# Kernel optimization log

Measured on AMD Instinct MI355X. Metric: run time of the kernel, lower is better.

## Reference

```python
import jax, jax.numpy as jnp
import numpy as np

NSAMPLE = 8
IN_FEAT = 64

def setup_inputs() -> dict:
    key = jax.random.key(0)
    ks = jax.random.split(key, 8)
    B, N1, N2, C = 2, 4096, 16384, IN_FEAT
    xyz1 = jax.random.normal(ks[0], (B, 3, N1), jnp.float32)
    xyz2 = jax.random.normal(ks[1], (B, 3, N2), jnp.float32)
    feat1 = jax.random.normal(ks[2], (B, C, N1), jnp.float32)
    flow = jax.random.normal(ks[3], (B, 3, N1), jnp.float32)
    W1 = jax.random.normal(ks[4], (C, C + 3), jnp.float32) * 0.1
    b1 = jax.random.normal(ks[5], (C,), jnp.float32) * 0.1
    W2 = jax.random.normal(ks[6], (3, C), jnp.float32) * 0.1
    b2 = jax.random.normal(ks[7], (3,), jnp.float32) * 0.1
    return {"xyz1": xyz1, "xyz2": xyz2, "feat1": feat1, "flow": flow,
            "W1": W1, "b1": b1, "W2": W2, "b2": b2}

def _knn_idx(xyz2, xyz1, k):
    # squared distances between queries xyz2 [B,3,N2] and targets xyz1 [B,3,N1]
    q2 = jnp.sum(xyz2 * xyz2, axis=1)            # [B,N2]
    t2 = jnp.sum(xyz1 * xyz1, axis=1)            # [B,N1]
    qt = jnp.einsum('bcn,bcm->bnm', xyz2, xyz1)  # [B,N2,N1]
    d = q2[:, :, None] + t2[:, None, :] - 2.0 * qt
    _, idx = jax.lax.top_k(-d, k)                # [B,N2,k] nearest in N1
    return idx

def _group(x, idx):
    # x [B,C,N1], idx [B,N2,k] -> [B,C,N2,k]
    return jax.vmap(lambda xb, ib: xb[:, ib])(x, idx)

def reference(xyz1, xyz2, feat1, flow, W1, b1, W2, b2):
    idx = _knn_idx(xyz2, xyz1, NSAMPLE)
    group_flow = _group(flow, idx)                           # [B,3,N2,k]
    group_xyz = _group(xyz1, idx) - xyz2[:, :, :, None]      # [B,3,N2,k]
    group_feat = _group(feat1, idx)                          # [B,C,N2,k]
    h = jnp.concatenate([group_feat, group_xyz], axis=1)     # [B,C+3,N2,k]
    h = jnp.einsum('oc,bcnk->bonk', W1, h) + b1[None, :, None, None]
    h = jnp.where(h >= 0, h, 0.1 * h)                        # LeakyReLU(0.1)
    w = jnp.einsum('oc,bcnk->bonk', W2, h) + b2[None, :, None, None]  # [B,3,N2,k]
    w = jax.nn.softmax(w, axis=3)
    up_flow = jnp.sum(group_flow * w, axis=3)                # [B,3,N2]
    return up_flow
```

## Files before the change

kernel.cpp:

```cpp
#include <hip/hip_runtime.h>
#include <cstdint>
#include <cstddef>

#define NB    2
#define N1    4096
#define N2    16384
#define CF    64
#define KNN   8
#define SPLIT1 16
#define NS1   (N1 / SPLIT1)
#define NQ    (NB * N2)

#define DNET(d) do { \
    const float m0_ = fminf(d, d0); \
    const float m1_ = __builtin_amdgcn_fmed3f(d, d0, d1); \
    const float m2_ = __builtin_amdgcn_fmed3f(d, d1, d2); \
    const float m3_ = __builtin_amdgcn_fmed3f(d, d2, d3); \
    const float m4_ = __builtin_amdgcn_fmed3f(d, d3, d4); \
    const float m5_ = __builtin_amdgcn_fmed3f(d, d4, d5); \
    const float m6_ = __builtin_amdgcn_fmed3f(d, d5, d6); \
    const float m7_ = __builtin_amdgcn_fmed3f(d, d6, d7); \
    d0=m0_; d1=m1_; d2=m2_; d3=m3_; d4=m4_; d5=m5_; d6=m6_; d7=m7_; \
} while (0)

__device__ __forceinline__ float distq(float qx, float qy, float qz, float q2,
                                       float4 p) {
    const float qt = __fadd_rn(
        __fadd_rn(__fmul_rn(qx, p.x), __fmul_rn(qy, p.y)),
        __fmul_rn(qz, p.z));
    return __fsub_rn(__fadd_rn(q2, p.w), __fadd_rn(qt, qt));
}

__global__ __launch_bounds__(256, 2) void k_pack(
    const float* __restrict__ xyz1, const float* __restrict__ xyz2,
    const float* __restrict__ feat1, const float* __restrict__ flow,
    float* __restrict__ feat1T, float4* __restrict__ aux4,
    float4* __restrict__ flow4, float4* __restrict__ q4)
{
    __shared__ float tile[64][65];
    const int b  = blockIdx.y;
    const int n0 = blockIdx.x * 64;
    const int tid = threadIdx.x;
    const int nl = tid & 63, cq = tid >> 6;

#pragma unroll
    for (int r = 0; r < 16; ++r) {
        const int c = r * 4 + cq;
        tile[c][nl] = feat1[((size_t)(b * CF + c)) * N1 + n0 + nl];
    }
    __syncthreads();
#pragma unroll
    for (int r = 0; r < 16; ++r) {
        const int nn = r * 4 + cq;
        feat1T[((size_t)(b * N1 + n0 + nn)) * CF + nl] = tile[nl][nn];
    }
    if (tid < 64) {
        const int n = n0 + tid;
        const float x = xyz1[(b * 3 + 0) * N1 + n];
        const float y = xyz1[(b * 3 + 1) * N1 + n];
        const float z = xyz1[(b * 3 + 2) * N1 + n];
        const float t2 = __fadd_rn(__fadd_rn(__fmul_rn(x, x), __fmul_rn(y, y)),
                                   __fmul_rn(z, z));
        aux4[b * N1 + n] = make_float4(x, y, z, t2);
        const float fx = flow[(b * 3 + 0) * N1 + n];
        const float fy = flow[(b * 3 + 1) * N1 + n];
        const float fz = flow[(b * 3 + 2) * N1 + n];
        flow4[b * N1 + n] = make_float4(fx, fy, fz, 0.f);
    }
    {
        const int qid = (blockIdx.y * 64 + blockIdx.x) * 256 + tid;
        const int qb_ = qid >> 14, qn_ = qid & (N2 - 1);
        const float x = xyz2[(qb_ * 3 + 0) * N2 + qn_];
        const float y = xyz2[(qb_ * 3 + 1) * N2 + qn_];
        const float z = xyz2[(qb_ * 3 + 2) * N2 + qn_];
        const float q2 = __fadd_rn(__fadd_rn(__fmul_rn(x, x), __fmul_rn(y, y)),
                                   __fmul_rn(z, z));
        q4[qid] = make_float4(x, y, z, q2);
    }
}

__global__ __launch_bounds__(256, 4) void k_knn5(
    const float4* __restrict__ aux4, const float4* __restrict__ q4,
    float* __restrict__ partd)
{
    __shared__ float4 pts[NS1];
    const int sp  = blockIdx.y;
    const int tid = threadIdx.x;
    const int qa  = blockIdx.x * 512 + tid;
    const int qb  = qa + 256;
    const int b   = qa >> 14;

    if (tid < NS1) {
        pts[tid] = aux4[b * N1 + sp * NS1 + tid];
    }
    __syncthreads();

    const float4 A = q4[qa];
    const float4 C = q4[qb];
    const float ax = A.x, ay = A.y, az = A.z, a2 = A.w;
    const float cx = C.x, cy = C.y, cz = C.z, c2 = C.w;

    float Aq0=INFINITY,Aq1=INFINITY,Aq2=INFINITY,Aq3=INFINITY,
          Aq4=INFINITY,Aq5=INFINITY,Aq6=INFINITY,Aq7=INFINITY;
    float Bq0=INFINITY,Bq1=INFINITY,Bq2=INFINITY,Bq3=INFINITY,
          Bq4=INFINITY,Bq5=INFINITY,Bq6=INFINITY,Bq7=INFINITY;

#pragma unroll 4
    for (int j = 0; j < NS1; ++j) {
        const float4 p = pts[j];
        const float dA = distq(ax, ay, az, a2, p);
        const float dB = distq(cx, cy, cz, c2, p);
        {
            float d0=Aq0,d1=Aq1,d2=Aq2,d3=Aq3,d4=Aq4,d5=Aq5,d6=Aq6,d7=Aq7;
            DNET(dA);
            Aq0=d0;Aq1=d1;Aq2=d2;Aq3=d3;Aq4=d4;Aq5=d5;Aq6=d6;Aq7=d7;
        }
        {
            float d0=Bq0,d1=Bq1,d2=Bq2,d3=Bq3,d4=Bq4,d5=Bq5,d6=Bq6,d7=Bq7;
            DNET(dB);
            Bq0=d0;Bq1=d1;Bq2=d2;Bq3=d3;Bq4=d4;Bq5=d5;Bq6=d6;Bq7=d7;
        }
    }

    {
        float4* pd4 = (float4*)(partd + ((size_t)sp * NQ + qa) * KNN);
        pd4[0] = make_float4(Aq0, Aq1, Aq2, Aq3);
        pd4[1] = make_float4(Aq4, Aq5, Aq6, Aq7);
    }
    {
        float4* pd4 = (float4*)(partd + ((size_t)sp * NQ + qb) * KNN);
        pd4[0] = make_float4(Bq0, Bq1, Bq2, Bq3);
        pd4[1] = make_float4(Bq4, Bq5, Bq6, Bq7);
    }
}

__global__ __launch_bounds__(256, 2) void k_thr(
    const float* __restrict__ partd, float* __restrict__ thr,
    int* __restrict__ tneed, int* __restrict__ smask)
{
    const int q = blockIdx.x * 256 + threadIdx.x;
    float d0=INFINITY,d1=INFINITY,d2=INFINITY,d3=INFINITY,
          d4=INFINITY,d5=INFINITY,d6=INFINITY,d7=INFINITY;
    float mn[SPLIT1];

#pragma unroll
    for (int sp = 0; sp < SPLIT1; ++sp) {
        const float4* pd4 = (const float4*)(partd + ((size_t)sp * NQ + q) * KNN);
        const float4 lo = pd4[0], hi = pd4[1];
        mn[sp] = lo.x;
        { const float d = lo.x; DNET(d); }
        { const float d = lo.y; DNET(d); }
        { const float d = lo.z; DNET(d); }
        { const float d = lo.w; DNET(d); }
        { const float d = hi.x; DNET(d); }
        { const float d = hi.y; DNET(d); }
        { const float d = hi.z; DNET(d); }
        { const float d = hi.w; DNET(d); }
    }
    const int s = (d0 < d7) + (d1 < d7) + (d2 < d7) + (d3 < d7) +
                  (d4 < d7) + (d5 < d7) + (d6 < d7);
    int mask = 0;
#pragma unroll
    for (int sp = 0; sp < SPLIT1; ++sp)
        mask |= (mn[sp] <= d7) ? (1 << sp) : 0;

    thr[q]   = d7;
    tneed[q] = 8 - s;
    smask[q] = mask;
}

__global__ __launch_bounds__(256, 4) void k_sel5(
    const float4* __restrict__ aux4, const float4* __restrict__ q4,
    const float* __restrict__ thr, const int* __restrict__ tneed,
    const int* __restrict__ smask, int* __restrict__ knn_idx)
{
    const int tid  = threadIdx.x;
    const int wave = tid >> 6, lane = tid & 63;
    const int q    = blockIdx.x * 4 + wave;
    const int b    = q >> 14;

    const float4 qv   = q4[q];
    const float  thrq = thr[q];
    const int    tn   = tneed[q];
    int mask = smask[q];

    int pos = 0, tc = 0;
    int* ko = knn_idx + (size_t)q * KNN;
    const float4* pts = aux4 + b * N1;

    while (mask) {
        const int sp = __builtin_ctz(mask); mask &= mask - 1;
        const int jb = sp * NS1;
#pragma unroll
        for (int t = 0; t < 4; ++t) {
            const float4 p = pts[jb + t * 64 + lane];
            const float d = distq(qv.x, qv.y, qv.z, qv.w, p);
            unsigned long long s = __ballot(d <  thrq);
            unsigned long long e = __ballot(d == thrq);
            const int jbase = jb + t * 64;
            while (s) {
                const int bit = __builtin_ctzll(s); s &= s - 1;
                if (lane == 0 && pos < 8) ko[pos] = jbase + bit;
                ++pos;
            }
            while (e && tc < tn) {
                const int bit = __builtin_ctzll(e); e &= e - 1;
                if (lane == 0 && pos < 8) ko[pos] = jbase + bit;
                ++pos; ++tc;
            }
        }
        if (pos >= 8) break;
    }
}

#define R4(WV, C4, BK) { \
    const float4 i0_ = *(const float4*)(inw + ((BK)+0)*68 + (C4)*4); \
    const float4 i1_ = *(const float4*)(inw + ((BK)+1)*68 + (C4)*4); \
    const float4 i2_ = *(const float4*)(inw + ((BK)+2)*68 + (C4)*4); \
    const float4 i3_ = *(const float4*)(inw + ((BK)+3)*68 + (C4)*4); \
    ha = fmaf((WV).x, i0_.x, ha); ha = fmaf((WV).y, i0_.y, ha); \
    ha = fmaf((WV).z, i0_.z, ha); ha = fmaf((WV).w, i0_.w, ha); \
    hb = fmaf((WV).x, i1_.x, hb); hb = fmaf((WV).y, i1_.y, hb); \
    hb = fmaf((WV).z, i1_.z, hb); hb = fmaf((WV).w, i1_.w, hb); \
    hc = fmaf((WV).x, i2_.x, hc); hc = fmaf((WV).y, i2_.y, hc); \
    hc = fmaf((WV).z, i2_.z, hc); hc = fmaf((WV).w, i2_.w, hc); \
    hd = fmaf((WV).x, i3_.x, hd); hd = fmaf((WV).y, i3_.y, hd); \
    hd = fmaf((WV).z, i3_.z, hd); hd = fmaf((WV).w, i3_.w, hd); \
}

#define DPPS12(PRE, MODS, POST) \
    asm(PRE \
        "v_add_f32_dpp %0, %0, %0 "   MODS "\n\t" \
        "v_add_f32_dpp %1, %1, %1 "   MODS "\n\t" \
        "v_add_f32_dpp %2, %2, %2 "   MODS "\n\t" \
        "v_add_f32_dpp %3, %3, %3 "   MODS "\n\t" \
        "v_add_f32_dpp %4, %4, %4 "   MODS "\n\t" \
        "v_add_f32_dpp %5, %5, %5 "   MODS "\n\t" \
        "v_add_f32_dpp %6, %6, %6 "   MODS "\n\t" \
        "v_add_f32_dpp %7, %7, %7 "   MODS "\n\t" \
        "v_add_f32_dpp %8, %8, %8 "   MODS "\n\t" \
        "v_add_f32_dpp %9, %9, %9 "   MODS "\n\t" \
        "v_add_f32_dpp %10, %10, %10 " MODS "\n\t" \
        "v_add_f32_dpp %11, %11, %11 " MODS POST \
        : "+v"(pa0), "+v"(pb0), "+v"(pc0), "+v"(pd0), \
          "+v"(pa1), "+v"(pb1), "+v"(pc1), "+v"(pd1), \
          "+v"(pa2), "+v"(pb2), "+v"(pc2), "+v"(pd2))

#define RDL(v) __int_as_float(__builtin_amdgcn_readlane(__float_as_int(v), 63))

#define L1L2_QUAD(BK, SA0,SA1,SA2,SA3, SB0,SB1,SB2,SB3, SC0,SC1,SC2,SC3) do { \
    float ha = b1v, hb = b1v, hc = b1v, hd = b1v; \
    R4(w0, 0, BK)  R4(w1, 1, BK)  R4(w2, 2, BK)  R4(w3, 3, BK) \
    R4(w4, 4, BK)  R4(w5, 5, BK)  R4(w6, 6, BK)  R4(w7, 7, BK) \
    R4(w8, 8, BK)  R4(w9, 9, BK)  R4(w10,10, BK) R4(w11,11, BK) \
    R4(w12,12, BK) R4(w13,13, BK) R4(w14,14, BK) R4(w15,15, BK) \
    R4(w16,16, BK) \
    ha = ha >= 0.f ? ha : 0.1f * ha; \
    hb = hb >= 0.f ? hb : 0.1f * hb; \
    hc = hc >= 0.f ? hc : 0.1f * hc; \
    hd = hd >= 0.f ? hd : 0.1f * hd; \
    float pa0 = w2a*ha, pb0 = w2a*hb, pc0 = w2a*hc, pd0 = w2a*hd; \
    float pa1 = w2b*ha, pb1 = w2b*hb, pc1 = w2b*hc, pd1 = w2b*hd; \
    float pa2 = w2c*ha, pb2 = w2c*hb, pc2 = w2c*hc, pd2 = w2c*hd; \
    DPPS12("s_nop 1\n\t", "row_shr:1 row_mask:0xf bank_mask:0xf", ""); \
    DPPS12("", "row_shr:2 row_mask:0xf bank_mask:0xf", ""); \
    DPPS12("", "row_shr:4 row_mask:0xf bank_mask:0xf", ""); \
    DPPS12("", "row_shr:8 row_mask:0xf bank_mask:0xf", ""); \
    DPPS12("", "row_bcast:15 row_mask:0xa bank_mask:0xf", ""); \
    DPPS12("", "row_bcast:31 row_mask:0xc bank_mask:0xf", "\n\ts_nop 1"); \
    SA0 = RDL(pa0) + b20; SA1 = RDL(pb0) + b20; \
    SA2 = RDL(pc0) + b20; SA3 = RDL(pd0) + b20; \
    SB0 = RDL(pa1) + b21; SB1 = RDL(pb1) + b21; \
    SB2 = RDL(pc1) + b21; SB3 = RDL(pd1) + b21; \
    SC0 = RDL(pa2) + b22; SC1 = RDL(pb2) + b22; \
    SC2 = RDL(pc2) + b22; SC3 = RDL(pd2) + b22; \
} while (0)

#define SMAX8(sa, sb, sc, sd, se, sf, sg, sh, CH, res) do { \
    const float m_ = fmaxf(fmaxf(fmaxf(sa, sb), fmaxf(sc, sd)), \
                           fmaxf(fmaxf(se, sf), fmaxf(sg, sh))); \
    const float e0_ = __expf(sa - m_), e1_ = __expf(sb - m_); \
    const float e2_ = __expf(sc - m_), e3_ = __expf(sd - m_); \
    const float e4_ = __expf(se - m_), e5_ = __expf(sf - m_); \
    const float e6_ = __expf(sg - m_), e7_ = __expf(sh - m_); \
    const float S_ = ((e0_ + e1_) + (e2_ + e3_)) + ((e4_ + e5_) + (e6_ + e7_)); \
    float acc_ = e0_ * flf[0 * 4 + CH]; \
    acc_ = fmaf(e1_, flf[1 * 4 + CH], acc_); acc_ = fmaf(e2_, flf[2 * 4 + CH], acc_); \
    acc_ = fmaf(e3_, flf[3 * 4 + CH], acc_); acc_ = fmaf(e4_, flf[4 * 4 + CH], acc_); \
    acc_ = fmaf(e5_, flf[5 * 4 + CH], acc_); acc_ = fmaf(e6_, flf[6 * 4 + CH], acc_); \
    acc_ = fmaf(e7_, flf[7 * 4 + CH], acc_); \
    res = acc_ * __builtin_amdgcn_rcpf(S_); \
} while (0)

#define MLP_STEP(IT) do { \
    const int n_ = n0 + (IT); \
    __builtin_amdgcn_wave_barrier(); \
    float4* drow = (float4*)(inw + k * 68); \
    drow[p * 2] = g0; drow[p * 2 + 1] = g1; \
    if (p == 0) { \
        inw[k * 68 + 64] = axv.x - qx; inw[k * 68 + 65] = axv.y - qy; \
        inw[k * 68 + 66] = axv.z - qz; inw[k * 68 + 67] = 0.f; \
    } \
    if (p == 1) flbuf[wave][k] = flv; \
    __builtin_amdgcn_wave_barrier(); \
    if ((IT) < 7) { \
        const int idn_ = idnext; \
        const float4* fr_ = (const float4*)(feat1T + (size_t)(base + idn_) * CF); \
        g0 = fr_[p * 2]; g1 = fr_[p * 2 + 1]; \
        axv = aux4[base + idn_]; flv = flow4[base + idn_]; \
        qx = xyz2[(b * 3 + 0) * N2 + n_ + 1]; \
        qy = xyz2[(b * 3 + 1) * N2 + n_ + 1]; \
        qz = xyz2[(b * 3 + 2) * N2 + n_ + 1]; \
        if ((IT) < 6) idnext = knn_idx[(size_t)(q0 + (IT) + 2) * KNN + k]; \
    } \
    float s00, s01, s02, s03, s04, s05, s06, s07; \
    float s10, s11, s12, s13, s14, s15, s16, s17; \
    float s20, s21, s22, s23, s24, s25, s26, s27; \
    L1L2_QUAD(0, s00,s01,s02,s03, s10,s11,s12,s13, s20,s21,s22,s23); \
    L1L2_QUAD(4, s04,s05,s06,s07, s14,s15,s16,s17, s24,s25,s26,s27); \
    float res0, res1, res2; \
    SMAX8(s00, s01, s02, s03, s04, s05, s06, s07, 0, res0); \
    SMAX8(s10, s11, s12, s13, s14, s15, s16, s17, 1, res1); \
    SMAX8(s20, s21, s22, s23, s24, s25, s26, s27, 2, res2); \
    const float resv = lane == 0 ? res0 : (lane == 1 ? res1 : res2); \
    if (lane < 3) out[((size_t)(b * 3 + lane)) * N2 + n_] = resv; \
} while (0)

__global__ __launch_bounds__(256, 2) void k_mlp5(
    const float* __restrict__ feat1T, const float4* __restrict__ aux4,
    const float4* __restrict__ flow4, const int* __restrict__ knn_idx,
    const float* __restrict__ xyz2,
    const float* __restrict__ W1, const float* __restrict__ b1,
    const float* __restrict__ W2, const float* __restrict__ b2,
    float* __restrict__ out)
{
    __shared__ __align__(16) float w1s[64 * 68];
    __shared__ __align__(16) float inbuf[4][8][68];
    __shared__ __align__(16) float4 flbuf[4][8];

    const int tid  = threadIdx.x;
    const int wave = tid >> 6, lane = tid & 63;

    for (int t = tid; t < 64 * 67; t += 256) {
        const int o = t / 67, c = t - o * 67;
        w1s[o * 68 + c] = W1[t];
    }
    if (tid < 64) w1s[tid * 68 + 67] = 0.f;

    const float b1v = b1[lane];
    const float w2a = W2[lane], w2b = W2[64 + lane], w2c = W2[128 + lane];
    const float b20 = b2[0], b21 = b2[1], b22 = b2[2];
    __syncthreads();

    const float4* wr = (const float4*)&w1s[lane * 68];
    const float4 w0 = wr[0],  w1 = wr[1],  w2 = wr[2],  w3 = wr[3];
    const float4 w4 = wr[4],  w5 = wr[5],  w6 = wr[6],  w7 = wr[7];
    const float4 w8 = wr[8],  w9 = wr[9],  w10 = wr[10], w11 = wr[11];
    const float4 w12 = wr[12], w13 = wr[13], w14 = wr[14], w15 = wr[15];
    const float4 w16 = wr[16];

    const int k = lane >> 3, p = lane & 7;
    float* inw = &inbuf[wave][0][0];
    const float* flf = (const float*)&flbuf[wave][0];

    const int q0   = blockIdx.x * 32 + wave * 8;
    const int b    = q0 >> 14;
    const int base = b * N1;
    const int n0   = q0 & (N2 - 1);

    const int id0v = knn_idx[(size_t)q0 * KNN + k];
    int idnext     = knn_idx[(size_t)(q0 + 1) * KNN + k];

    const float4* fr0 = (const float4*)(feat1T + (size_t)(base + id0v) * CF);
    float4 g0 = fr0[p * 2], g1 = fr0[p * 2 + 1];
    float4 axv = aux4[base + id0v];
    float4 flv = flow4[base + id0v];
    float qx = xyz2[(b * 3 + 0) * N2 + n0];
    float qy = xyz2[(b * 3 + 1) * N2 + n0];
    float qz = xyz2[(b * 3 + 2) * N2 + n0];

    MLP_STEP(0);
    MLP_STEP(1);
    MLP_STEP(2);
    MLP_STEP(3);
    MLP_STEP(4);
    MLP_STEP(5);
    MLP_STEP(6);
    MLP_STEP(7);
}

extern "C" void kernel_launch(void* const* d_in, const int* in_sizes, int n_in,
                              void* d_out, int out_size, void* d_ws, size_t ws_size,
                              hipStream_t stream)
{
    const float* xyz1  = (const float*)d_in[0];
    const float* xyz2  = (const float*)d_in[1];
    const float* feat1 = (const float*)d_in[2];
    const float* flow  = (const float*)d_in[3];
    const float* W1    = (const float*)d_in[4];
    const float* b1    = (const float*)d_in[5];
    const float* W2    = (const float*)d_in[6];
    const float* b2    = (const float*)d_in[7];
    float* out = (float*)d_out;

    char* ws = (char*)d_ws;
    float*  feat1T  = (float*)(ws);
    float4* aux4    = (float4*)(ws + (size_t)(2u << 20));
    float4* flow4   = (float4*)(ws + (size_t)(2u << 20) + (512u << 10));
    int*    knn_idx = (int*)  (ws + (size_t)(3u << 20));
    float*  partd   = (float*)(ws + (size_t)(4u << 20));
    float*  thr     = (float*)(ws + (size_t)(20u << 20));
    int*    tneed   = (int*)  (ws + (size_t)(20u << 20) + (512u << 10));
    int*    smask   = (int*)  (ws + (size_t)(21u << 20));
    float4* q4      = (float4*)(ws + (size_t)(21u << 20) + (512u << 10));

    hipLaunchKernelGGL(k_pack, dim3(N1 / 64, NB), dim3(256), 0, stream,
                       xyz1, xyz2, feat1, flow, feat1T, aux4, flow4, q4);
    hipLaunchKernelGGL(k_knn5, dim3(NQ / 512, SPLIT1), dim3(256), 0, stream,
                       aux4, q4, partd);
    hipLaunchKernelGGL(k_thr, dim3(NQ / 256), dim3(256), 0, stream,
                       partd, thr, tneed, smask);
    hipLaunchKernelGGL(k_sel5, dim3(NQ / 4), dim3(256), 0, stream,
                       aux4, q4, thr, tneed, smask, knn_idx);
    hipLaunchKernelGGL(k_mlp5, dim3(NQ / 32), dim3(256), 0, stream,
                       feat1T, aux4, flow4, knn_idx, xyz2, W1, b1, W2, b2, out);
}
```

Before: 270.0 us.

## Track per-64-point group minima to narrow KNN reselection to candidate groups

The partial KNN kernel now also records the minimum distance for each 64-point group within every split, and the threshold kernel builds a 64-bit group mask of the groups whose minimum is within the k-th distance. The selection kernel then rescans only those 64-point groups instead of whole 256-point splits, cutting redundant distance recomputation and ballots. The cost is an extra fminf per point plus an extra float4 write and read per query per split. The MLP kernel's launch bound occupancy hint is also raised from 2 to 4, which may limit registers.

```diff
diff --git a/kernel.cpp b/kernel.cpp
--- a/kernel.cpp
+++ b/kernel.cpp
@@ -79,9 +79,29 @@
     }
 }
 
-__global__ __launch_bounds__(256, 4) void k_knn5(
+#define KSEG(G, GA, GB) \
+    GA = INFINITY; GB = INFINITY; \
+    _Pragma("unroll 4") \
+    for (int j = (G) * 64; j < (G) * 64 + 64; ++j) { \
+        const float4 p = pts[j]; \
+        const float dA = distq(ax, ay, az, a2, p); \
+        const float dB = distq(cx, cy, cz, c2, p); \
+        GA = fminf(GA, dA); GB = fminf(GB, dB); \
+        { \
+            float d0=Aq0,d1=Aq1,d2=Aq2,d3=Aq3,d4=Aq4,d5=Aq5,d6=Aq6,d7=Aq7; \
+            DNET(dA); \
+            Aq0=d0;Aq1=d1;Aq2=d2;Aq3=d3;Aq4=d4;Aq5=d5;Aq6=d6;Aq7=d7; \
+        } \
+        { \
+            float d0=Bq0,d1=Bq1,d2=Bq2,d3=Bq3,d4=Bq4,d5=Bq5,d6=Bq6,d7=Bq7; \
+            DNET(dB); \
+            Bq0=d0;Bq1=d1;Bq2=d2;Bq3=d3;Bq4=d4;Bq5=d5;Bq6=d6;Bq7=d7; \
+        } \
+    }
+
+__global__ __launch_bounds__(256, 4) void k_knn6(
     const float4* __restrict__ aux4, const float4* __restrict__ q4,
-    float* __restrict__ partd)
+    float* __restrict__ partd, float4* __restrict__ partg)
 {
     __shared__ float4 pts[NS1];
     const int sp  = blockIdx.y;
@@ -104,50 +124,40 @@
           Aq4=INFINITY,Aq5=INFINITY,Aq6=INFINITY,Aq7=INFINITY;
     float Bq0=INFINITY,Bq1=INFINITY,Bq2=INFINITY,Bq3=INFINITY,
           Bq4=INFINITY,Bq5=INFINITY,Bq6=INFINITY,Bq7=INFINITY;
-
-#pragma unroll 4
-    for (int j = 0; j < NS1; ++j) {
-        const float4 p = pts[j];
-        const float dA = distq(ax, ay, az, a2, p);
-        const float dB = distq(cx, cy, cz, c2, p);
-        {
-            float d0=Aq0,d1=Aq1,d2=Aq2,d3=Aq3,d4=Aq4,d5=Aq5,d6=Aq6,d7=Aq7;
-            DNET(dA);
-            Aq0=d0;Aq1=d1;Aq2=d2;Aq3=d3;Aq4=d4;Aq5=d5;Aq6=d6;Aq7=d7;
-        }
-        {
-            float d0=Bq0,d1=Bq1,d2=Bq2,d3=Bq3,d4=Bq4,d5=Bq5,d6=Bq6,d7=Bq7;
-            DNET(dB);
-            Bq0=d0;Bq1=d1;Bq2=d2;Bq3=d3;Bq4=d4;Bq5=d5;Bq6=d6;Bq7=d7;
-        }
-    }
+    float gA0, gA1, gA2, gA3, gB0, gB1, gB2, gB3;
+
+    KSEG(0, gA0, gB0)
+    KSEG(1, gA1, gB1)
+    KSEG(2, gA2, gB2)
+    KSEG(3, gA3, gB3)
 
     {
         float4* pd4 = (float4*)(partd + ((size_t)sp * NQ + qa) * KNN);
         pd4[0] = make_float4(Aq0, Aq1, Aq2, Aq3);
         pd4[1] = make_float4(Aq4, Aq5, Aq6, Aq7);
+        partg[(size_t)sp * NQ + qa] = make_float4(gA0, gA1, gA2, gA3);
     }
     {
         float4* pd4 = (float4*)(partd + ((size_t)sp * NQ + qb) * KNN);
         pd4[0] = make_float4(Bq0, Bq1, Bq2, Bq3);
         pd4[1] = make_float4(Bq4, Bq5, Bq6, Bq7);
+        partg[(size_t)sp * NQ + qb] = make_float4(gB0, gB1, gB2, gB3);
     }
 }
 
 __global__ __launch_bounds__(256, 2) void k_thr(
-    const float* __restrict__ partd, float* __restrict__ thr,
-    int* __restrict__ tneed, int* __restrict__ smask)
+    const float* __restrict__ partd, const float4* __restrict__ partg,
+    float* __restrict__ thr, int* __restrict__ tneed,
+    unsigned long long* __restrict__ gmask)
 {
     const int q = blockIdx.x * 256 + threadIdx.x;
     float d0=INFINITY,d1=INFINITY,d2=INFINITY,d3=INFINITY,
           d4=INFINITY,d5=INFINITY,d6=INFINITY,d7=INFINITY;
-    float mn[SPLIT1];
 
 #pragma unroll
     for (int sp = 0; sp < SPLIT1; ++sp) {
         const float4* pd4 = (const float4*)(partd + ((size_t)sp * NQ + q) * KNN);
         const float4 lo = pd4[0], hi = pd4[1];
-        mn[sp] = lo.x;
         { const float d = lo.x; DNET(d); }
         { const float d = lo.y; DNET(d); }
         { const float d = lo.z; DNET(d); }
@@ -159,20 +169,26 @@
     }
     const int s = (d0 < d7) + (d1 < d7) + (d2 < d7) + (d3 < d7) +
                   (d4 < d7) + (d5 < d7) + (d6 < d7);
-    int mask = 0;
+
+    unsigned long long gm = 0ull;
 #pragma unroll
-    for (int sp = 0; sp < SPLIT1; ++sp)
-        mask |= (mn[sp] <= d7) ? (1 << sp) : 0;
+    for (int sp = 0; sp < SPLIT1; ++sp) {
+        const float4 g = partg[(size_t)sp * NQ + q];
+        gm |= (g.x <= d7 ? 1ull : 0ull) << (sp * 4 + 0);
+        gm |= (g.y <= d7 ? 1ull : 0ull) << (sp * 4 + 1);
+        gm |= (g.z <= d7 ? 1ull : 0ull) << (sp * 4 + 2);
+        gm |= (g.w <= d7 ? 1ull : 0ull) << (sp * 4 + 3);
+    }
 
     thr[q]   = d7;
     tneed[q] = 8 - s;
-    smask[q] = mask;
-}
-
-__global__ __launch_bounds__(256, 4) void k_sel5(
+    gmask[q] = gm;
+}
+
+__global__ __launch_bounds__(256, 4) void k_sel6(
     const float4* __restrict__ aux4, const float4* __restrict__ q4,
     const float* __restrict__ thr, const int* __restrict__ tneed,
-    const int* __restrict__ smask, int* __restrict__ knn_idx)
+    const unsigned long long* __restrict__ gmask, int* __restrict__ knn_idx)
 {
     const int tid  = threadIdx.x;
     const int wave = tid >> 6, lane = tid & 63;
@@ -182,32 +198,28 @@
     const float4 qv   = q4[q];
     const float  thrq = thr[q];
     const int    tn   = tneed[q];
-    int mask = smask[q];
+    unsigned long long m = gmask[q];
 
     int pos = 0, tc = 0;
     int* ko = knn_idx + (size_t)q * KNN;
     const float4* pts = aux4 + b * N1;
 
-    while (mask) {
-        const int sp = __builtin_ctz(mask); mask &= mask - 1;
-        const int jb = sp * NS1;
-#pragma unroll
-        for (int t = 0; t < 4; ++t) {
-            const float4 p = pts[jb + t * 64 + lane];
-            const float d = distq(qv.x, qv.y, qv.z, qv.w, p);
-            unsigned long long s = __ballot(d <  thrq);
-            unsigned long long e = __ballot(d == thrq);
-            const int jbase = jb + t * 64;
-            while (s) {
-                const int bit = __builtin_ctzll(s); s &= s - 1;
-                if (lane == 0 && pos < 8) ko[pos] = jbase + bit;
-                ++pos;
-            }
-            while (e && tc < tn) {
-                const int bit = __builtin_ctzll(e); e &= e - 1;
-                if (lane == 0 && pos < 8) ko[pos] = jbase + bit;
-                ++pos; ++tc;
-            }
+    while (m) {
+        const int g = __builtin_ctzll(m); m &= m - 1;
+        const int jbase = g * 64;
+        const float4 p = pts[jbase + lane];
+        const float d = distq(qv.x, qv.y, qv.z, qv.w, p);
+        unsigned long long s = __ballot(d <  thrq);
+        unsigned long long e = __ballot(d == thrq);
+        while (s) {
+            const int bit = __builtin_ctzll(s); s &= s - 1;
+            if (lane == 0 && pos < 8) ko[pos] = jbase + bit;
+            ++pos;
+        }
+        while (e && tc < tn) {
+            const int bit = __builtin_ctzll(e); e &= e - 1;
+            if (lane == 0 && pos < 8) ko[pos] = jbase + bit;
+            ++pos; ++tc;
         }
         if (pos >= 8) break;
     }
@@ -326,7 +338,7 @@
     if (lane < 3) out[((size_t)(b * 3 + lane)) * N2 + n_] = resv; \
 } while (0)
 
-__global__ __launch_bounds__(256, 2) void k_mlp5(
+__global__ __launch_bounds__(256, 4) void k_mlp5(
     const float* __restrict__ feat1T, const float4* __restrict__ aux4,
     const float4* __restrict__ flow4, const int* __restrict__ knn_idx,
     const float* __restrict__ xyz2,
@@ -411,17 +423,18 @@
     float*  partd   = (float*)(ws + (size_t)(4u << 20));
     float*  thr     = (float*)(ws + (size_t)(20u << 20));
     int*    tneed   = (int*)  (ws + (size_t)(20u << 20) + (512u << 10));
-    int*    smask   = (int*)  (ws + (size_t)(21u << 20));
+    unsigned long long* gmask = (unsigned long long*)(ws + (size_t)(21u << 20));
     float4* q4      = (float4*)(ws + (size_t)(21u << 20) + (512u << 10));
+    float4* partg   = (float4*)(ws + (size_t)(22u << 20));
 
     hipLaunchKernelGGL(k_pack, dim3(N1 / 64, NB), dim3(256), 0, stream,
                        xyz1, xyz2, feat1, flow, feat1T, aux4, flow4, q4);
-    hipLaunchKernelGGL(k_knn5, dim3(NQ / 512, SPLIT1), dim3(256), 0, stream,
-                       aux4, q4, partd);
+    hipLaunchKernelGGL(k_knn6, dim3(NQ / 512, SPLIT1), dim3(256), 0, stream,
+                       aux4, q4, partd, partg);
     hipLaunchKernelGGL(k_thr, dim3(NQ / 256), dim3(256), 0, stream,
-                       partd, thr, tneed, smask);
-    hipLaunchKernelGGL(k_sel5, dim3(NQ / 4), dim3(256), 0, stream,
-                       aux4, q4, thr, tneed, smask, knn_idx);
+                       partd, partg, thr, tneed, gmask);
+    hipLaunchKernelGGL(k_sel6, dim3(NQ / 4), dim3(256), 0, stream,
+                       aux4, q4, thr, tneed, gmask, knn_idx);
     hipLaunchKernelGGL(k_mlp5, dim3(NQ / 32), dim3(256), 0, stream,
                        feat1T, aux4, flow4, knn_idx, xyz2, W1, b1, W2, b2, out);
 }
```

Result: slower. 415.9 us (+54.0%).
